# Kernel tuning notes

Measured on AMD Instinct MI355X. Metric: run time of the kernel, lower is better.

The kernel has to match this reference:

```python
import jax, jax.numpy as jnp
import numpy as np

NUM_HEADS = 16
THETA = 10000.0


def _rope(x, pos, theta):
    # x: [b, h, s, d_k] with d_k even; rotate interleaved pairs (even, odd)
    d = x.shape[-1]
    inv_freq = theta ** (-jnp.arange(0, d, 2, dtype=jnp.float32) / d)  # [d/2]
    ang = pos.astype(jnp.float32)[:, None] * inv_freq                  # [s, d/2]
    cos = jnp.cos(ang)[None, None]                                     # [1,1,s,d/2]
    sin = jnp.sin(ang)[None, None]
    x1 = x[..., 0::2]
    x2 = x[..., 1::2]
    r1 = x1 * cos - x2 * sin
    r2 = x1 * sin + x2 * cos
    return jnp.stack([r1, r2], axis=-1).reshape(x.shape)


def setup_inputs() -> dict:
    key = jax.random.key(0)
    ks = jax.random.split(key, 5)
    B, S, D = 2, 2048, 1024
    x = jax.random.normal(ks[0], (B, S, D), dtype=jnp.float32)
    scale = 0.02
    Wq = jax.random.normal(ks[1], (D, D), dtype=jnp.float32) * scale
    Wk = jax.random.normal(ks[2], (D, D), dtype=jnp.float32) * scale
    Wv = jax.random.normal(ks[3], (D, D), dtype=jnp.float32) * scale
    Wo = jax.random.normal(ks[4], (D, D), dtype=jnp.float32) * scale
    return {"x": x, "Wq": Wq, "Wk": Wk, "Wv": Wv, "Wo": Wo}


def reference(x, Wq, Wk, Wv, Wo):
    B, S, D = x.shape
    H = NUM_HEADS
    dk = D // H
    # QKV projections (bias-free Linear: y = x @ W^T, W is [out, in])
    q = (x @ Wq.T).reshape(B, S, H, dk).transpose(0, 2, 1, 3)  # [b,h,s,dk]
    k = (x @ Wk.T).reshape(B, S, H, dk).transpose(0, 2, 1, 3)
    v = (x @ Wv.T).reshape(B, S, H, dk).transpose(0, 2, 1, 3)
    pos = jnp.arange(S)
    q = _rope(q, pos, THETA)
    k = _rope(k, pos, THETA)
    # naive masked SDPA, causal mask
    scores = jnp.einsum('bhqd,bhkd->bhqk', q, k) / (dk ** 0.5)
    causal = jnp.tril(jnp.ones((S, S), dtype=bool))
    scores = jnp.where(causal, scores, -jnp.inf)
    attn = jax.nn.softmax(scores, axis=-1)
    out = jnp.einsum('bhqk,bhkd->bhqd', attn, v)
    out = out.transpose(0, 2, 1, 3).reshape(B, S, D)
    return out @ Wo.T
```

## Files before the change

kernel.cpp:

```cpp
#include <hip/hip_runtime.h>
#include <hip/hip_bf16.h>
#include <stdint.h>

typedef __bf16 bf16;
typedef __bf16 bf16x8 __attribute__((ext_vector_type(8)));
typedef float f32x4 __attribute__((ext_vector_type(4)));
typedef float f32x16 __attribute__((ext_vector_type(16)));

#define B_ 2
#define S_ 2048
#define D_ 1024
#define H_ 16
#define DK 64
#define M_ 4096

__device__ __forceinline__ void gload_lds16(const void* g, void* l) {
  __builtin_amdgcn_global_load_lds(
      (const __attribute__((address_space(1))) uint32_t*)(uintptr_t)g,
      (__attribute__((address_space(3))) uint32_t*)(uintptr_t)l, 16, 0, 0);
}

__device__ __forceinline__ uint32_t pkbf(float a, float b) {
  union { uint32_t u; struct { bf16 x, y; } s; } r;
  r.s.x = (bf16)a; r.s.y = (bf16)b;
  return r.u;
}

struct alignas(8) B4s { bf16 a, b, c, d; };

__global__ __launch_bounds__(256) void cvt_all_kernel(
    const float* __restrict__ x, const float* __restrict__ wq, const float* __restrict__ wk,
    const float* __restrict__ wv, const float* __restrict__ wo,
    bf16* __restrict__ xb, bf16* __restrict__ wqb, bf16* __restrict__ wkb,
    bf16* __restrict__ wvb, bf16* __restrict__ wob) {
  int i = blockIdx.x * 256 + threadIdx.x;
  const float* src;
  bf16* dst;
  int off;
  if (i < 1048576) { src = x; dst = xb; off = i; }
  else if (i < 1310720) { src = wq; dst = wqb; off = i - 1048576; }
  else if (i < 1572864) { src = wk; dst = wkb; off = i - 1310720; }
  else if (i < 1835008) { src = wv; dst = wvb; off = i - 1572864; }
  else { src = wo; dst = wob; off = i - 1835008; }
  float4 v = reinterpret_cast<const float4*>(src)[off];
  B4s o{(bf16)v.x, (bf16)v.y, (bf16)v.z, (bf16)v.w};
  reinterpret_cast<B4s*>(dst)[off] = o;
}

template <int MODE>
__global__ __launch_bounds__(256) void gemm_kernel(
    const bf16* __restrict__ A,
    const bf16* __restrict__ W0, const bf16* __restrict__ W1, const bf16* __restrict__ W2,
    bf16* __restrict__ q_out, bf16* __restrict__ k_out, bf16* __restrict__ v_out,
    float* __restrict__ c_out) {
  constexpr int BK = 64;
  constexpr int BM = (MODE == 0) ? 128 : 64;
  constexpr int FM = (MODE == 0) ? 4 : 2;
  constexpr int NT = (MODE == 0) ? 24 : 8;
  constexpr int PERX = (MODE == 0) ? 96 : 64;
  __shared__ bf16 Alds[BM * BK];
  __shared__ bf16 Blds[128 * BK];
  const int tid = threadIdx.x;
  const int w = tid >> 6, l = tid & 63;
  const int lr = l & 15, lg = l >> 4;
  const int lin = (blockIdx.x & 7) * PERX + (blockIdx.x >> 3);
  const int m0 = (lin / NT) * BM;
  const int nt = lin % NT;
  const bf16* W;
  int n0;
  const int rt = (MODE == 0) ? (nt >> 3) : 0;
  if (MODE == 0) {
    W = rt == 0 ? W0 : (rt == 1 ? W1 : W2);
    n0 = (nt & 7) * 128;
  } else {
    W = W0;
    n0 = nt * 128;
  }
  const int K = 1024;
  const int wm = (MODE == 0) ? (w >> 1) * 64 : (w & 1) * 32;
  const int wn = (MODE == 0) ? (w & 1) * 64 : (w >> 1) * 64;
  const int srow = w * 8 + (l >> 3);
  const int scol = (l & 7) * 8;
  f32x4 acc[FM][4] = {};
  for (int k0 = 0; k0 < K; k0 += BK) {
    const bf16* Ab = A + (size_t)m0 * K + k0;
    const bf16* Bb = W + (size_t)n0 * K + k0;
#pragma unroll
    for (int c = 0; c < BM / 32; ++c)
      gload_lds16(Ab + (size_t)(c * 32 + srow) * K + scol, Alds + (c * 32 + w * 8) * BK);
#pragma unroll
    for (int c = 0; c < 4; ++c)
      gload_lds16(Bb + (size_t)(c * 32 + srow) * K + scol, Blds + (c * 32 + w * 8) * BK);
    __syncthreads();
#pragma unroll
    for (int kk = 0; kk < 2; ++kk) {
      bf16x8 af[FM], bfr[4];
#pragma unroll
      for (int f = 0; f < FM; ++f)
        af[f] = *reinterpret_cast<const bf16x8*>(Alds + (wm + f * 16 + lr) * BK + kk * 32 + lg * 8);
#pragma unroll
      for (int f = 0; f < 4; ++f)
        bfr[f] = *reinterpret_cast<const bf16x8*>(Blds + (wn + f * 16 + lr) * BK + kk * 32 + lg * 8);
#pragma unroll
      for (int fm = 0; fm < FM; ++fm)
#pragma unroll
        for (int fn = 0; fn < 4; ++fn)
          acc[fm][fn] = __builtin_amdgcn_mfma_f32_16x16x32_bf16(af[fm], bfr[fn], acc[fm][fn], 0, 0, 0);
    }
    __syncthreads();
  }
#pragma unroll
  for (int fm = 0; fm < FM; ++fm)
#pragma unroll
    for (int fn = 0; fn < 4; ++fn)
#pragma unroll
      for (int r = 0; r < 4; ++r) {
        int m = m0 + wm + fm * 16 + lg * 4 + r;
        int n = n0 + wn + fn * 16 + lr;
        float v = acc[fm][fn][r];
        if (MODE == 0) {
          bf16* dst = rt == 0 ? q_out : (rt == 1 ? k_out : v_out);
          int h = n >> 6, d = n & 63;
          int b = m >> 11, s = m & 2047;
          dst[(((size_t)b * H_ + h) * S_ + s) * DK + d] = (bf16)v;
        } else {
          c_out[(size_t)m * D_ + n] = v;
        }
      }
}

__global__ __launch_bounds__(256) void rope_kernel(bf16* __restrict__ Q, bf16* __restrict__ K) {
  const int NG = 32 * 2048 * 8;
  int idx = blockIdx.x * 256 + threadIdx.x;
  bf16* X = Q;
  float sc = 0.18033688f;
  if (idx >= NG) { X = K; idx -= NG; sc = 1.0f; }
  int g = idx & 7;
  int s = (idx >> 3) & 2047;
  int bh = idx >> 14;
  size_t off = ((size_t)bh * S_ + s) * DK + g * 8;
  bf16x8 v = *reinterpret_cast<const bf16x8*>(X + off);
  bf16x8 o;
  const float c0 = -0.4152410118609203f;
  float fs = (float)s;
#pragma unroll
  for (int p = 0; p < 4; ++p) {
    int i = g * 4 + p;
    float ang = fs * exp2f((float)i * c0);
    float sn = __sinf(ang), cs = __cosf(ang);
    float x1 = (float)v[2 * p], x2 = (float)v[2 * p + 1];
    o[2 * p]     = (bf16)((x1 * cs - x2 * sn) * sc);
    o[2 * p + 1] = (bf16)((x1 * sn + x2 * cs) * sc);
  }
  *reinterpret_cast<bf16x8*>(X + off) = o;
}

__global__ __launch_bounds__(256, 4) void attn_kernel(
    const bf16* __restrict__ Q, const bf16* __restrict__ K, const bf16* __restrict__ V,
    bf16* __restrict__ O) {
  __shared__ __align__(16) char smem[40960];
  bf16* K3 = (bf16*)smem;
  bf16* Vt2 = (bf16*)smem + 12288;
  float* MG = (float*)smem;
  const int tid = threadIdx.x;
  const int w = tid >> 6, l = tid & 63;
  const int ql = l & 31, h = l >> 5;
  const int kh = w >> 1, qh = w & 1;
  const int qt = 31 - (int)(blockIdx.x >> 5);
  const int bh = blockIdx.x & 31;
  const size_t base = (size_t)bh * S_ * DK;

  const size_t qrow = base + (size_t)(qt * 64 + qh * 32 + ql) * DK;
  bf16x8 qf[4];
#pragma unroll
  for (int t = 0; t < 4; ++t)
    qf[t] = *reinterpret_cast<const bf16x8*>(Q + qrow + t * 16 + h * 8);

  float l_run = 0.f;
  f32x16 o0 = {}, o1 = {};

  auto stageK = [&](int kt, int buf) {
#pragma unroll
    for (int c = 0; c < 2; ++c) {
      int row = c * 32 + w * 8 + (l >> 3);
      int col = ((l & 7) * 8) ^ ((row & 7) * 8);
      gload_lds16(K + base + (size_t)(kt * 64 + row) * DK + col,
                  K3 + buf * 4096 + c * 2048 + w * 512);
    }
  };
  auto loadV = [&](int kt, bf16x8 (&pv)[2]) {
    const bf16* vp = V + base + (size_t)(kt * 64 + l) * DK + w * 16;
    pv[0] = *reinterpret_cast<const bf16x8*>(vp);
    pv[1] = *reinterpret_cast<const bf16x8*>(vp + 8);
  };
  auto writeV = [&](int vb, const bf16x8 (&pv)[2]) {
    bf16* Vt = Vt2 + vb * 4096;
#pragma unroll
    for (int j = 0; j < 8; ++j) {
      Vt[(w * 16 + j) * 64 + (l ^ (j * 8))] = pv[0][j];
      Vt[(w * 16 + 8 + j) * 64 + (l ^ (j * 8))] = pv[1][j];
    }
  };

  {
    bf16x8 pv[2];
    loadV(0, pv);
    stageK(0, 0);
    if (qt >= 1) stageK(1, 1);
    writeV(0, pv);
    if (qt >= 1) {
      asm volatile("s_waitcnt vmcnt(2)" ::: "memory");
    } else {
      asm volatile("s_waitcnt vmcnt(0)" ::: "memory");
    }
    asm volatile("s_waitcnt lgkmcnt(0)" ::: "memory");
    __builtin_amdgcn_sched_barrier(0);
    __builtin_amdgcn_s_barrier();
    __builtin_amdgcn_sched_barrier(0);
  }

  const int swzd = (ql & 7) * 8;
  const int keyA = kh * 32 + ql;
  const int limq = qh * 32 + ql;
  bf16x8 pvv[2];
  int kb = 0, kb2 = 2;

  for (int kt = 0; kt <= qt; ++kt) {
    const int vb = kt & 1;
    const bool pre = kt < qt;
    const bool pre2 = kt + 2 <= qt;
    const bool lastt = (kt == qt);
    const bool skipw = lastt && (kh == 1) && (qh == 0);
    if (pre) loadV(kt + 1, pvv);
    if (pre2) stageK(kt + 2, kb2);
    if (!skipw) {
      f32x16 ss = {};
      __builtin_amdgcn_s_setprio(1);
#pragma unroll
      for (int t = 0; t < 4; ++t) {
        bf16x8 kf = *reinterpret_cast<const bf16x8*>(
            K3 + kb * 4096 + keyA * 64 + ((t * 16 + h * 8) ^ ((keyA & 7) * 8)));
        ss = __builtin_amdgcn_mfma_f32_32x32x16_bf16(kf, qf[t], ss, 0, 0, 0);
      }
      __builtin_amdgcn_s_setprio(0);
      if (lastt) {
#pragma unroll
        for (int r = 0; r < 16; ++r) {
          int kl = kh * 32 + (r & 3) + 8 * (r >> 2) + 4 * h;
          if (kl > limq) ss[r] = -INFINITY;
        }
      }
      float t0 = 0.f, t1 = 0.f, t2 = 0.f, t3 = 0.f;
#pragma unroll
      for (int r = 0; r < 16; r += 4) {
        float p0 = exp2f(ss[r]);
        float p1 = exp2f(ss[r + 1]);
        float p2 = exp2f(ss[r + 2]);
        float p3 = exp2f(ss[r + 3]);
        ss[r] = p0; ss[r + 1] = p1; ss[r + 2] = p2; ss[r + 3] = p3;
        t0 += p0; t1 += p1; t2 += p2; t3 += p3;
      }
      l_run += (t0 + t1) + (t2 + t3);
      uint32_t Wq_[4][2];
#pragma unroll
      for (int g = 0; g < 4; ++g) {
        Wq_[g][0] = pkbf(ss[4 * g + 0], ss[4 * g + 1]);
        Wq_[g][1] = pkbf(ss[4 * g + 2], ss[4 * g + 3]);
      }
      __builtin_amdgcn_s_setprio(1);
#pragma unroll
      for (int ks = 0; ks < 2; ++ks) {
        uint32_t a0 = Wq_[2 * ks][0], a1 = Wq_[2 * ks][1];
        uint32_t b0 = Wq_[2 * ks + 1][0], b1 = Wq_[2 * ks + 1][1];
        uint32_t sxa0 = (uint32_t)__shfl_xor((int)a0, 32);
        uint32_t sxa1 = (uint32_t)__shfl_xor((int)a1, 32);
        uint32_t sxb0 = (uint32_t)__shfl_xor((int)b0, 32);
        uint32_t sxb1 = (uint32_t)__shfl_xor((int)b1, 32);
        union { uint32_t u[4]; bf16x8 v; } pa;
        pa.u[0] = h ? sxb0 : a0;
        pa.u[1] = h ? sxb1 : a1;
        pa.u[2] = h ? b0 : sxa0;
        pa.u[3] = h ? b1 : sxa1;
        int col = (kh * 32 + ks * 16 + h * 8) ^ swzd;
        const bf16* Vt = Vt2 + vb * 4096;
        bf16x8 v0 = *reinterpret_cast<const bf16x8*>(&Vt[ql * 64 + col]);
        bf16x8 v1 = *reinterpret_cast<const bf16x8*>(&Vt[(32 + ql) * 64 + col]);
        o0 = __builtin_amdgcn_mfma_f32_32x32x16_bf16(pa.v, v0, o0, 0, 0, 0);
        o1 = __builtin_amdgcn_mfma_f32_32x32x16_bf16(pa.v, v1, o1, 0, 0, 0);
      }
      __builtin_amdgcn_s_setprio(0);
    }
    if (pre) writeV(vb ^ 1, pvv);
    asm volatile("s_waitcnt vmcnt(2)" ::: "memory");
    asm volatile("s_waitcnt lgkmcnt(0)" ::: "memory");
    __builtin_amdgcn_sched_barrier(0);
    __builtin_amdgcn_s_barrier();
    __builtin_amdgcn_sched_barrier(0);
    kb = (kb == 2) ? 0 : kb + 1;
    kb2 = (kb2 == 2) ? 0 : kb2 + 1;
  }

  l_run += __shfl_xor(l_run, 32);
  __syncthreads();
  if (kh == 1) {
    int off = (qh * 64 + l) * 33;
    MG[off] = l_run;
#pragma unroll
    for (int r = 0; r < 16; ++r) {
      MG[off + 1 + r] = o0[r];
      MG[off + 17 + r] = o1[r];
    }
  }
  __syncthreads();
  if (kh == 0) {
    int off = (qh * 64 + l) * 33;
    float inv = 1.0f / (l_run + MG[off]);
    const int b = bh >> 4, hd = bh & 15;
#pragma unroll
    for (int r = 0; r < 16; ++r) {
      int rowl = (r & 3) + 8 * (r >> 2) + 4 * h;
      float invr = __shfl(inv, rowl);
      int qr = qt * 64 + qh * 32 + rowl;
      size_t ooff = ((size_t)b * S_ + qr) * D_ + hd * 64;
      O[ooff + ql] = (bf16)((o0[r] + MG[off + 1 + r]) * invr);
      O[ooff + 32 + ql] = (bf16)((o1[r] + MG[off + 17 + r]) * invr);
    }
  }
}

extern "C" void kernel_launch(void* const* d_in, const int* in_sizes, int n_in,
                              void* d_out, int out_size, void* d_ws, size_t ws_size,
                              hipStream_t stream) {
  const float* x  = (const float*)d_in[0];
  const float* Wq = (const float*)d_in[1];
  const float* Wk = (const float*)d_in[2];
  const float* Wv = (const float*)d_in[3];
  const float* Wo = (const float*)d_in[4];
  float* out = (float*)d_out;
  char* ws = (char*)d_ws;

  bf16* xb  = (bf16*)(ws + ((size_t)0 << 20));
  bf16* wqb = (bf16*)(ws + ((size_t)8 << 20));
  bf16* wkb = (bf16*)(ws + ((size_t)10 << 20));
  bf16* wvb = (bf16*)(ws + ((size_t)12 << 20));
  bf16* wob = (bf16*)(ws + ((size_t)14 << 20));
  bf16* Qb  = (bf16*)(ws + ((size_t)16 << 20));
  bf16* Kb  = (bf16*)(ws + ((size_t)24 << 20));
  bf16* Vb  = (bf16*)(ws + ((size_t)32 << 20));
  bf16* Ob  = (bf16*)(ws + ((size_t)40 << 20));

  cvt_all_kernel<<<8192, 256, 0, stream>>>(x, Wq, Wk, Wv, Wo, xb, wqb, wkb, wvb, wob);
  gemm_kernel<0><<<768, 256, 0, stream>>>(xb, wqb, wkb, wvb, Qb, Kb, Vb, nullptr);
  rope_kernel<<<4096, 256, 0, stream>>>(Qb, Kb);
  attn_kernel<<<1024, 256, 0, stream>>>(Qb, Kb, Vb, Ob);
  gemm_kernel<1><<<512, 256, 0, stream>>>(Ob, wob, nullptr, nullptr, nullptr, nullptr,
                                          nullptr, out);
}
```

Measured before the change: 116.5 us.

## Switch GEMM to 32x32x16 MFMA with XOR-swizzled LDS layout

Replaces the 16x16x32 bf16 MFMA tiles in the projection GEMMs with 32x32x16 MFMA tiles. Loads from global to LDS now use an XOR swizzle on the column, and the fragment reads undo it, which is meant to avoid LDS bank conflicts. The epilogue index mapping is rewritten to match the 32x32 accumulator layout. It also adds a launch-bounds occupancy hint of 3 blocks. The larger MFMA tile should cut the number of LDS fragment reads per FLOP, but it raises accumulator register pressure.

```diff
diff --git a/kernel.cpp b/kernel.cpp
--- a/kernel.cpp
+++ b/kernel.cpp
@@ -48,21 +48,21 @@
 }
 
 template <int MODE>
-__global__ __launch_bounds__(256) void gemm_kernel(
+__global__ __launch_bounds__(256, 3) void gemm_kernel(
     const bf16* __restrict__ A,
     const bf16* __restrict__ W0, const bf16* __restrict__ W1, const bf16* __restrict__ W2,
     bf16* __restrict__ q_out, bf16* __restrict__ k_out, bf16* __restrict__ v_out,
     float* __restrict__ c_out) {
   constexpr int BK = 64;
   constexpr int BM = (MODE == 0) ? 128 : 64;
-  constexpr int FM = (MODE == 0) ? 4 : 2;
+  constexpr int AM = (MODE == 0) ? 2 : 1;
   constexpr int NT = (MODE == 0) ? 24 : 8;
   constexpr int PERX = (MODE == 0) ? 96 : 64;
   __shared__ bf16 Alds[BM * BK];
   __shared__ bf16 Blds[128 * BK];
   const int tid = threadIdx.x;
   const int w = tid >> 6, l = tid & 63;
-  const int lr = l & 15, lg = l >> 4;
+  const int l31 = l & 31, hh = l >> 5;
   const int lin = (blockIdx.x & 7) * PERX + (blockIdx.x >> 3);
   const int m0 = (lin / NT) * BM;
   const int nt = lin % NT;
@@ -80,8 +80,9 @@
   const int wm = (MODE == 0) ? (w >> 1) * 64 : (w & 1) * 32;
   const int wn = (MODE == 0) ? (w & 1) * 64 : (w >> 1) * 64;
   const int srow = w * 8 + (l >> 3);
-  const int scol = (l & 7) * 8;
-  f32x4 acc[FM][4] = {};
+  const int scol = ((l & 7) * 8) ^ (((l >> 3) & 7) * 8);
+  const int swz = (l & 7) * 8;
+  f32x16 acc[AM][2] = {};
   for (int k0 = 0; k0 < K; k0 += BK) {
     const bf16* Ab = A + (size_t)m0 * K + k0;
     const bf16* Bb = W + (size_t)n0 * K + k0;
@@ -92,32 +93,38 @@
     for (int c = 0; c < 4; ++c)
       gload_lds16(Bb + (size_t)(c * 32 + srow) * K + scol, Blds + (c * 32 + w * 8) * BK);
     __syncthreads();
-#pragma unroll
-    for (int kk = 0; kk < 2; ++kk) {
-      bf16x8 af[FM], bfr[4];
-#pragma unroll
-      for (int f = 0; f < FM; ++f)
-        af[f] = *reinterpret_cast<const bf16x8*>(Alds + (wm + f * 16 + lr) * BK + kk * 32 + lg * 8);
-#pragma unroll
-      for (int f = 0; f < 4; ++f)
-        bfr[f] = *reinterpret_cast<const bf16x8*>(Blds + (wn + f * 16 + lr) * BK + kk * 32 + lg * 8);
-#pragma unroll
-      for (int fm = 0; fm < FM; ++fm)
-#pragma unroll
-        for (int fn = 0; fn < 4; ++fn)
-          acc[fm][fn] = __builtin_amdgcn_mfma_f32_16x16x32_bf16(af[fm], bfr[fn], acc[fm][fn], 0, 0, 0);
-    }
+    bf16x8 af[AM][4], bfr[2][4];
+#pragma unroll
+    for (int am = 0; am < AM; ++am)
+#pragma unroll
+      for (int t = 0; t < 4; ++t)
+        af[am][t] = *reinterpret_cast<const bf16x8*>(
+            Alds + (wm + am * 32 + l31) * BK + ((t * 16 + hh * 8) ^ swz));
+#pragma unroll
+    for (int bn = 0; bn < 2; ++bn)
+#pragma unroll
+      for (int t = 0; t < 4; ++t)
+        bfr[bn][t] = *reinterpret_cast<const bf16x8*>(
+            Blds + (wn + bn * 32 + l31) * BK + ((t * 16 + hh * 8) ^ swz));
+#pragma unroll
+    for (int t = 0; t < 4; ++t)
+#pragma unroll
+      for (int am = 0; am < AM; ++am)
+#pragma unroll
+        for (int bn = 0; bn < 2; ++bn)
+          acc[am][bn] = __builtin_amdgcn_mfma_f32_32x32x16_bf16(af[am][t], bfr[bn][t],
+                                                               acc[am][bn], 0, 0, 0);
     __syncthreads();
   }
 #pragma unroll
-  for (int fm = 0; fm < FM; ++fm)
-#pragma unroll
-    for (int fn = 0; fn < 4; ++fn)
-#pragma unroll
-      for (int r = 0; r < 4; ++r) {
-        int m = m0 + wm + fm * 16 + lg * 4 + r;
-        int n = n0 + wn + fn * 16 + lr;
-        float v = acc[fm][fn][r];
+  for (int am = 0; am < AM; ++am)
+#pragma unroll
+    for (int bn = 0; bn < 2; ++bn)
+#pragma unroll
+      for (int r = 0; r < 16; ++r) {
+        int m = m0 + wm + am * 32 + (r & 3) + 8 * (r >> 2) + 4 * hh;
+        int n = n0 + wn + bn * 32 + l31;
+        float v = acc[am][bn][r];
         if (MODE == 0) {
           bf16* dst = rt == 0 ? q_out : (rt == 1 ? k_out : v_out);
           int h = n >> 6, d = n & 63;
```

Measured after the change: 107.9 us. 7.4% less time.
